# Performance work log

Hardware: AMD Instinct MI355X
Metric: run time of the kernel (lower is better)

Reference implementation:

```python
import jax, jax.numpy as jnp
import numpy as np

N_NODES = 50000
N_EDGES = 400000
NUM_INPUT = 3703
NUM_DIM = 256
NUM_OUT = 6


def setup_inputs() -> dict:
    key = jax.random.key(0)
    k = jax.random.split(key, 8)
    x = jax.random.normal(k[0], (N_NODES, NUM_INPUT), dtype=jnp.float32)
    edge_src = jax.random.randint(k[1], (N_EDGES,), 0, N_NODES, dtype=jnp.int32)
    edge_dst = jax.random.randint(k[2], (N_EDGES,), 0, N_NODES, dtype=jnp.int32)
    edge_weight = jax.random.uniform(k[3], (N_EDGES,), dtype=jnp.float32)
    W1 = jax.random.normal(k[4], (NUM_INPUT, NUM_DIM), dtype=jnp.float32) * (1.0 / np.sqrt(NUM_INPUT))
    b1 = jnp.zeros((NUM_DIM,), dtype=jnp.float32)
    W2 = jax.random.normal(k[5], (NUM_DIM, NUM_OUT), dtype=jnp.float32) * (1.0 / np.sqrt(NUM_DIM))
    b2 = jnp.zeros((NUM_OUT,), dtype=jnp.float32)
    return {"x": x, "edge_src": edge_src, "edge_dst": edge_dst,
            "edge_weight": edge_weight, "W1": W1, "b1": b1, "W2": W2, "b2": b2}


def _gcn_layer(h, W, b, src, dst, w):
    # support = h @ W  (dense transform), then sparse adj matmul via gather+segment_sum
    support = h @ W                              # [N, d_out]
    msg = support[src] * w[:, None]              # [E, d_out]
    agg = jax.ops.segment_sum(msg, dst, num_segments=h.shape[0])  # [N, d_out]
    return agg + b


def reference(x, edge_src, edge_dst, edge_weight, W1, b1, W2, b2):
    h = _gcn_layer(x, W1, b1, edge_src, edge_dst, edge_weight)
    h = jax.nn.leaky_relu(h, negative_slope=0.01)  # matches F.leaky_relu default
    h = _gcn_layer(h, W2, b2, edge_src, edge_dst, edge_weight)
    return jax.nn.log_softmax(h, axis=1)
```

## Files before the change

kernel.cpp:

```cpp
#include <hip/hip_runtime.h>
#include <math.h>

#define N_NODES   50000
#define N_EDGES   400000
#define NUM_INPUT 3703
#define NUM_DIM   256
#define NUM_OUT   6

#define KPAD   3712
#define KTILES 116

typedef __attribute__((ext_vector_type(8))) short short8;
typedef __attribute__((ext_vector_type(4))) float f32x4;

static __device__ __forceinline__ unsigned short f2bf(float f) {
    unsigned u = __float_as_uint(f);
    u += 0x7fffu + ((u >> 16) & 1u);
    return (unsigned short)(u >> 16);
}
static __device__ __forceinline__ float bf2f(unsigned short h) {
    return __uint_as_float(((unsigned)h) << 16);
}

__global__ __launch_bounds__(256) void w1_split_kernel(
    const float* __restrict__ W1,
    unsigned short* __restrict__ Wh, unsigned short* __restrict__ Wl)
{
    int idx = blockIdx.x * 256 + threadIdx.x;
    if (idx >= NUM_DIM * KPAD) return;
    int col = idx / KPAD;
    int k   = idx - col * KPAD;
    float v = (k < NUM_INPUT) ? W1[(size_t)k * NUM_DIM + col] : 0.f;
    unsigned short h = f2bf(v);
    Wh[idx] = h;
    Wl[idx] = f2bf(v - bf2f(h));
}

__global__ __launch_bounds__(256) void deg_count_kernel(
    const int* __restrict__ dst, int* __restrict__ deg)
{
    int e = blockIdx.x * 256 + threadIdx.x;
    if (e >= N_EDGES) return;
    atomicAdd(&deg[dst[e]], 1);
}

__global__ __launch_bounds__(1024) void scan_kernel(
    const int* __restrict__ deg, int* __restrict__ row_ptr,
    int* __restrict__ cursor)
{
    __shared__ int buf[1024];
    __shared__ int carry_s;
    const int tid = threadIdx.x;
    if (tid == 0) carry_s = 0;
    __syncthreads();
    for (int base = 0; base < N_NODES; base += 1024) {
        const int i = base + tid;
        const int v = (i < N_NODES) ? deg[i] : 0;
        buf[tid] = v;
        __syncthreads();
#pragma unroll
        for (int off = 1; off < 1024; off <<= 1) {
            int t = (tid >= off) ? buf[tid - off] : 0;
            __syncthreads();
            buf[tid] += t;
            __syncthreads();
        }
        const int c = carry_s;
        if (i < N_NODES) {
            const int excl = c + buf[tid] - v;
            row_ptr[i] = excl;
            cursor[i]  = excl;
        }
        const int tot = buf[1023];
        __syncthreads();
        if (tid == 0) carry_s = c + tot;
        __syncthreads();
    }
    if (tid == 0) row_ptr[N_NODES] = carry_s;
}

__global__ __launch_bounds__(256) void fill_kernel(
    const int* __restrict__ dst, int* __restrict__ cursor,
    int* __restrict__ edge_idx)
{
    int e = blockIdx.x * 256 + threadIdx.x;
    if (e >= N_EDGES) return;
    int pos = atomicAdd(&cursor[dst[e]], 1);
    edge_idx[pos] = e;
}

__global__ __launch_bounds__(256) void gemm1_kernel(
    const float* __restrict__ x,
    const unsigned short* __restrict__ Wh, const unsigned short* __restrict__ Wl,
    float* __restrict__ support)
{
    __shared__ unsigned short Ah[64][32];
    __shared__ unsigned short Al[64][32];
    __shared__ unsigned short Bh[256][32];
    __shared__ unsigned short Bl[256][32];

    const int t    = threadIdx.x;
    const int lane = t & 63;
    const int wv   = t >> 6;
    const int m0   = blockIdx.x * 64;

    const int arow = t >> 2;
    const int akc  = t & 3;
    const int fr   = lane & 15;
    const int fg   = lane >> 4;

    const int gr   = m0 + arow;
    const bool rok = (gr < N_NODES);
    const float* xrow = x + (size_t)gr * NUM_INPUT + akc * 8;

    char* ah_dst = (char*)&Ah[0][0] + t * 16;
    char* al_dst = (char*)&Al[0][0] + t * 16;
    char* bh_dst = (char*)&Bh[0][0] + t * 16;
    char* bl_dst = (char*)&Bl[0][0] + t * 16;
    const int bcol0 = t >> 2;

    f32x4 acc[4][4];
#pragma unroll
    for (int i = 0; i < 4; ++i)
#pragma unroll
        for (int j = 0; j < 4; ++j) acc[i][j] = (f32x4){0.f, 0.f, 0.f, 0.f};

    for (int kt = 0; kt < KTILES; ++kt) {
        const int k0 = kt * 32;
        __syncthreads();

#pragma unroll
        for (int c = 0; c < 4; ++c) {
            const size_t goff = (size_t)(bcol0 + 64 * c) * KPAD + k0 + akc * 8;
            __builtin_amdgcn_global_load_lds(
                (const __attribute__((address_space(1))) void*)(Wh + goff),
                (__attribute__((address_space(3))) void*)(bh_dst + c * 4096),
                16, 0, 0);
            __builtin_amdgcn_global_load_lds(
                (const __attribute__((address_space(1))) void*)(Wl + goff),
                (__attribute__((address_space(3))) void*)(bl_dst + c * 4096),
                16, 0, 0);
        }

        float av[8];
#pragma unroll
        for (int j = 0; j < 8; ++j) {
            const int gk = k0 + akc * 8 + j;
            av[j] = (rok && gk < NUM_INPUT) ? xrow[k0 + j] : 0.f;
        }
        short8 vh, vl;
#pragma unroll
        for (int j = 0; j < 8; ++j) {
            const unsigned short h = f2bf(av[j]);
            vh[j] = (short)h;
            vl[j] = (short)f2bf(av[j] - bf2f(h));
        }
        *(short8*)ah_dst = vh;
        *(short8*)al_dst = vl;

        __syncthreads();

        short8 ahf[4], alf[4];
#pragma unroll
        for (int mb = 0; mb < 4; ++mb) {
            ahf[mb] = *(const short8*)&Ah[mb * 16 + fr][fg * 8];
            alf[mb] = *(const short8*)&Al[mb * 16 + fr][fg * 8];
        }
#pragma unroll
        for (int nb = 0; nb < 4; ++nb) {
            const int col = wv * 64 + nb * 16 + fr;
            const short8 bhf = *(const short8*)&Bh[col][fg * 8];
            const short8 blf = *(const short8*)&Bl[col][fg * 8];
#pragma unroll
            for (int mb = 0; mb < 4; ++mb) {
                acc[mb][nb] = __builtin_amdgcn_mfma_f32_16x16x32_bf16(
                    alf[mb], bhf, acc[mb][nb], 0, 0, 0);
                acc[mb][nb] = __builtin_amdgcn_mfma_f32_16x16x32_bf16(
                    ahf[mb], blf, acc[mb][nb], 0, 0, 0);
                acc[mb][nb] = __builtin_amdgcn_mfma_f32_16x16x32_bf16(
                    ahf[mb], bhf, acc[mb][nb], 0, 0, 0);
            }
        }
    }

#pragma unroll
    for (int mb = 0; mb < 4; ++mb) {
        const int row = m0 + mb * 16 + fg * 4;
#pragma unroll
        for (int r = 0; r < 4; ++r) {
            if (row + r < N_NODES) {
#pragma unroll
                for (int nb = 0; nb < 4; ++nb)
                    support[(size_t)(row + r) * NUM_DIM + wv * 64 + nb * 16 + fr] =
                        acc[mb][nb][r];
            }
        }
    }
}

__global__ __launch_bounds__(256) void agg1_fused_kernel(
    const float* __restrict__ support, const int* __restrict__ row_ptr,
    const int* __restrict__ edge_idx, const int* __restrict__ src,
    const float* __restrict__ w, const float* __restrict__ b1,
    const float* __restrict__ W2, float* __restrict__ support2)
{
    __shared__ float W2s[NUM_DIM][NUM_OUT];
    const int t = threadIdx.x;
#pragma unroll
    for (int j = 0; j < NUM_OUT; ++j) W2s[t][j] = W2[t * NUM_OUT + j];
    __syncthreads();

    const int node = blockIdx.x * 4 + (t >> 6);
    const int lane = t & 63;
    if (node >= N_NODES) return;

    const int p0 = row_ptr[node], p1 = row_ptr[node + 1];
    float4 acc = make_float4(0.f, 0.f, 0.f, 0.f);
    for (int p = p0; p < p1; ++p) {
        const int e = edge_idx[p];
        const float we = w[e];
        const float4 v = *(const float4*)&support[(size_t)src[e] * NUM_DIM + lane * 4];
        acc.x += v.x * we; acc.y += v.y * we;
        acc.z += v.z * we; acc.w += v.w * we;
    }
    const float4 bv = *(const float4*)&b1[lane * 4];
    float hv[4];
    hv[0] = acc.x + bv.x; hv[1] = acc.y + bv.y;
    hv[2] = acc.z + bv.z; hv[3] = acc.w + bv.w;
#pragma unroll
    for (int c = 0; c < 4; ++c) hv[c] = (hv[c] > 0.f) ? hv[c] : 0.01f * hv[c];

    float o[NUM_OUT];
#pragma unroll
    for (int j = 0; j < NUM_OUT; ++j) o[j] = 0.f;
#pragma unroll
    for (int c = 0; c < 4; ++c) {
        const int k = lane * 4 + c;
#pragma unroll
        for (int j = 0; j < NUM_OUT; ++j) o[j] += hv[c] * W2s[k][j];
    }
#pragma unroll
    for (int j = 0; j < NUM_OUT; ++j) {
#pragma unroll
        for (int off = 32; off > 0; off >>= 1)
            o[j] += __shfl_down(o[j], off);
    }
    if (lane == 0) {
#pragma unroll
        for (int j = 0; j < NUM_OUT; ++j)
            support2[(size_t)node * NUM_OUT + j] = o[j];
    }
}

__global__ __launch_bounds__(256) void agg2_fused_kernel(
    const float* __restrict__ support2, const int* __restrict__ row_ptr,
    const int* __restrict__ edge_idx, const int* __restrict__ src,
    const float* __restrict__ w, const float* __restrict__ b2,
    float* __restrict__ out)
{
    const int t    = threadIdx.x;
    const int node = blockIdx.x * 4 + (t >> 6);
    const int lane = t & 63;
    if (node >= N_NODES) return;

    const int p0 = row_ptr[node], p1 = row_ptr[node + 1];
    float o[NUM_OUT];
#pragma unroll
    for (int j = 0; j < NUM_OUT; ++j) o[j] = 0.f;
    for (int p = p0 + lane; p < p1; p += 64) {
        const int e = edge_idx[p];
        const float we = w[e];
        const float* sp = &support2[(size_t)src[e] * NUM_OUT];
#pragma unroll
        for (int j = 0; j < NUM_OUT; ++j) o[j] += sp[j] * we;
    }
#pragma unroll
    for (int j = 0; j < NUM_OUT; ++j) {
#pragma unroll
        for (int off = 32; off > 0; off >>= 1)
            o[j] += __shfl_down(o[j], off);
    }
    if (lane == 0) {
        float v[NUM_OUT];
        float m = -1e30f;
#pragma unroll
        for (int j = 0; j < NUM_OUT; ++j) {
            v[j] = o[j] + b2[j];
            m = fmaxf(m, v[j]);
        }
        float s = 0.f;
#pragma unroll
        for (int j = 0; j < NUM_OUT; ++j) s += expf(v[j] - m);
        const float ls = logf(s);
#pragma unroll
        for (int j = 0; j < NUM_OUT; ++j)
            out[(size_t)node * NUM_OUT + j] = v[j] - m - ls;
    }
}

extern "C" void kernel_launch(void* const* d_in, const int* in_sizes, int n_in,
                              void* d_out, int out_size, void* d_ws, size_t ws_size,
                              hipStream_t stream)
{
    const float* x   = (const float*)d_in[0];
    const int*   src = (const int*)  d_in[1];
    const int*   dst = (const int*)  d_in[2];
    const float* w   = (const float*)d_in[3];
    const float* W1  = (const float*)d_in[4];
    const float* b1  = (const float*)d_in[5];
    const float* W2  = (const float*)d_in[6];
    const float* b2  = (const float*)d_in[7];
    float* out = (float*)d_out;

    char* ws = (char*)d_ws;
    float*          support1 = (float*)(ws);
    float*          support2 = (float*)(ws + 51200000);
    unsigned short* W1t_hi   = (unsigned short*)(ws + 52400000);
    unsigned short* W1t_lo   = (unsigned short*)(ws + 54300544);
    int*            deg_cur  = (int*)(ws + 56201088);
    int*            row_ptr  = (int*)(ws + 56401088);
    int*            edge_idx = (int*)(ws + 56601092);

    hipMemsetAsync(deg_cur, 0, (size_t)N_NODES * sizeof(int), stream);

    deg_count_kernel<<<dim3((N_EDGES + 255) / 256), 256, 0, stream>>>(dst, deg_cur);
    scan_kernel<<<dim3(1), 1024, 0, stream>>>(deg_cur, row_ptr, deg_cur);
    fill_kernel<<<dim3((N_EDGES + 255) / 256), 256, 0, stream>>>(dst, deg_cur, edge_idx);

    w1_split_kernel<<<dim3((NUM_DIM * KPAD + 255) / 256), 256, 0, stream>>>(
        W1, W1t_hi, W1t_lo);
    gemm1_kernel<<<dim3((N_NODES + 63) / 64), 256, 0, stream>>>(
        x, W1t_hi, W1t_lo, support1);
    agg1_fused_kernel<<<dim3((N_NODES + 3) / 4), 256, 0, stream>>>(
        support1, row_ptr, edge_idx, src, w, b1, W2, support2);
    agg2_fused_kernel<<<dim3((N_NODES + 3) / 4), 256, 0, stream>>>(
        support2, row_ptr, edge_idx, src, w, b2, out);
}
```

Before: 1.667 ms.

## Double-buffer GEMM with pre-tiled swizzled W1 image and pre-sorted edge arrays

The W1 preprocessing now writes a per-k-tile, bank-swizzled hi/lo bf16 image so each GEMM tile is one contiguous block. The GEMM now double-buffers its LDS tiles, prefetching the next x and W tiles during the current MFMAs with one barrier per iteration, and splits the hi part by truncation. The CSR fill now stores src and weight in sorted order, removing the edge_idx indirection. Aggregation batches neighbour indices through wave shuffles with 4-way unrolled gathers, and the scan uses wave shuffles instead of a barrier-heavy LDS scan. These add LDS use (about 80KB per block, which may lower occupancy), and the truncated hi split changes rounding slightly.

```diff
diff --git a/kernel.cpp b/kernel.cpp
--- a/kernel.cpp
+++ b/kernel.cpp
@@ -13,27 +13,36 @@
 typedef __attribute__((ext_vector_type(8))) short short8;
 typedef __attribute__((ext_vector_type(4))) float f32x4;
 
-static __device__ __forceinline__ unsigned short f2bf(float f) {
+static __device__ __forceinline__ unsigned short f2bf_rne(float f) {
     unsigned u = __float_as_uint(f);
     u += 0x7fffu + ((u >> 16) & 1u);
     return (unsigned short)(u >> 16);
 }
-static __device__ __forceinline__ float bf2f(unsigned short h) {
-    return __uint_as_float(((unsigned)h) << 16);
-}
-
-__global__ __launch_bounds__(256) void w1_split_kernel(
-    const float* __restrict__ W1,
-    unsigned short* __restrict__ Wh, unsigned short* __restrict__ Wl)
-{
-    int idx = blockIdx.x * 256 + threadIdx.x;
-    if (idx >= NUM_DIM * KPAD) return;
-    int col = idx / KPAD;
-    int k   = idx - col * KPAD;
-    float v = (k < NUM_INPUT) ? W1[(size_t)k * NUM_DIM + col] : 0.f;
-    unsigned short h = f2bf(v);
-    Wh[idx] = h;
-    Wl[idx] = f2bf(v - bf2f(h));
+
+__global__ __launch_bounds__(256) void w1_img_kernel(
+    const float* __restrict__ W1, unsigned short* __restrict__ img)
+{
+    int cg = blockIdx.x * 256 + threadIdx.x;
+    if (cg >= KTILES * 1024) return;
+    int kt   = cg >> 10;
+    int cc   = cg & 1023;
+    int col  = cc >> 2;
+    int spos = cc & 3;
+    int slot = (spos - (col >> 1)) & 3;
+    int k0   = kt * 32 + slot * 8;
+    size_t base = (size_t)kt * 16384 + (size_t)cc * 8;
+    short8 vh, vl;
+#pragma unroll
+    for (int j = 0; j < 8; ++j) {
+        int k = k0 + j;
+        float v = (k < NUM_INPUT) ? W1[(size_t)k * NUM_DIM + col] : 0.f;
+        unsigned u = __float_as_uint(v);
+        vh[j] = (short)(u >> 16);
+        float rec = __uint_as_float(u & 0xffff0000u);
+        vl[j] = (short)f2bf_rne(v - rec);
+    }
+    *(short8*)(img + base)        = vh;
+    *(short8*)(img + base + 8192) = vl;
 }
 
 __global__ __launch_bounds__(256) void deg_count_kernel(
@@ -48,56 +57,61 @@
     const int* __restrict__ deg, int* __restrict__ row_ptr,
     int* __restrict__ cursor)
 {
-    __shared__ int buf[1024];
+    __shared__ int wsum[16];
     __shared__ int carry_s;
-    const int tid = threadIdx.x;
+    const int tid = threadIdx.x, lane = tid & 63, wid = tid >> 6;
     if (tid == 0) carry_s = 0;
     __syncthreads();
     for (int base = 0; base < N_NODES; base += 1024) {
         const int i = base + tid;
         const int v = (i < N_NODES) ? deg[i] : 0;
-        buf[tid] = v;
-        __syncthreads();
-#pragma unroll
-        for (int off = 1; off < 1024; off <<= 1) {
-            int t = (tid >= off) ? buf[tid - off] : 0;
-            __syncthreads();
-            buf[tid] += t;
-            __syncthreads();
-        }
-        const int c = carry_s;
-        if (i < N_NODES) {
-            const int excl = c + buf[tid] - v;
-            row_ptr[i] = excl;
-            cursor[i]  = excl;
-        }
-        const int tot = buf[1023];
-        __syncthreads();
-        if (tid == 0) carry_s = c + tot;
-        __syncthreads();
-    }
-    if (tid == 0) row_ptr[N_NODES] = carry_s;
+        int x = v;
+#pragma unroll
+        for (int off = 1; off < 64; off <<= 1) {
+            int y = __shfl_up(x, off);
+            if (lane >= off) x += y;
+        }
+        if (lane == 63) wsum[wid] = x;
+        __syncthreads();
+        if (wid == 0) {
+            int s = (lane < 16) ? wsum[lane] : 0;
+#pragma unroll
+            for (int off = 1; off < 16; off <<= 1) {
+                int y = __shfl_up(s, off);
+                if (lane >= off) s += y;
+            }
+            if (lane < 16) wsum[lane] = s;
+        }
+        __syncthreads();
+        const int wpre  = (wid == 0) ? 0 : wsum[wid - 1];
+        const int carry = carry_s;
+        const int incl  = carry + wpre + x;
+        if (i < N_NODES) { row_ptr[i] = incl - v; cursor[i] = incl - v; }
+        __syncthreads();
+        if (tid == 1023) carry_s = incl;
+        __syncthreads();
+    }
+    if (threadIdx.x == 0) row_ptr[N_NODES] = carry_s;
 }
 
 __global__ __launch_bounds__(256) void fill_kernel(
-    const int* __restrict__ dst, int* __restrict__ cursor,
-    int* __restrict__ edge_idx)
+    const int* __restrict__ dst, const int* __restrict__ src,
+    const float* __restrict__ w, int* __restrict__ cursor,
+    int* __restrict__ src_s, float* __restrict__ w_s)
 {
     int e = blockIdx.x * 256 + threadIdx.x;
     if (e >= N_EDGES) return;
     int pos = atomicAdd(&cursor[dst[e]], 1);
-    edge_idx[pos] = e;
+    src_s[pos] = src[e];
+    w_s[pos]   = w[e];
 }
 
 __global__ __launch_bounds__(256) void gemm1_kernel(
-    const float* __restrict__ x,
-    const unsigned short* __restrict__ Wh, const unsigned short* __restrict__ Wl,
+    const float* __restrict__ x, const unsigned short* __restrict__ Wimg,
     float* __restrict__ support)
 {
-    __shared__ unsigned short Ah[64][32];
-    __shared__ unsigned short Al[64][32];
-    __shared__ unsigned short Bh[256][32];
-    __shared__ unsigned short Bl[256][32];
+    __shared__ unsigned short Abuf[2][4096];
+    __shared__ unsigned short Bbuf[2][16384];
 
     const int t    = threadIdx.x;
     const int lane = t & 63;
@@ -111,13 +125,10 @@
 
     const int gr   = m0 + arow;
     const bool rok = (gr < N_NODES);
-    const float* xrow = x + (size_t)gr * NUM_INPUT + akc * 8;
-
-    char* ah_dst = (char*)&Ah[0][0] + t * 16;
-    char* al_dst = (char*)&Al[0][0] + t * 16;
-    char* bh_dst = (char*)&Bh[0][0] + t * 16;
-    char* bl_dst = (char*)&Bl[0][0] + t * 16;
-    const int bcol0 = t >> 2;
+    const float* xbase = x + (size_t)(rok ? gr : 0) * NUM_INPUT + akc * 8;
+
+    const int a_woff = arow * 32 + ((akc + (arow >> 1)) & 3) * 8;
+    const int aslot  = ((fg + (fr >> 1)) & 3) * 8;
 
     f32x4 acc[4][4];
 #pragma unroll
@@ -125,52 +136,68 @@
 #pragma unroll
         for (int j = 0; j < 4; ++j) acc[i][j] = (f32x4){0.f, 0.f, 0.f, 0.f};
 
+    float av[8];
+
+#pragma unroll
+    for (int j = 0; j < 8; ++j)
+        av[j] = rok ? xbase[j] : 0.f;
+    {
+        const unsigned short* wsrc = Wimg + (size_t)t * 8;
+        unsigned short* bdst = &Bbuf[0][t * 8];
+#pragma unroll
+        for (int r = 0; r < 8; ++r)
+            __builtin_amdgcn_global_load_lds(
+                (const __attribute__((address_space(1))) void*)(wsrc + r * 2048),
+                (__attribute__((address_space(3))) void*)(bdst + r * 2048),
+                16, 0, 0);
+    }
+    {
+        short8 vh, vl;
+#pragma unroll
+        for (int j = 0; j < 8; ++j) {
+            unsigned u = __float_as_uint(av[j]);
+            vh[j] = (short)(u >> 16);
+            float rec = __uint_as_float(u & 0xffff0000u);
+            vl[j] = (short)f2bf_rne(av[j] - rec);
+        }
+        *(short8*)(&Abuf[0][a_woff])        = vh;
+        *(short8*)(&Abuf[0][2048 + a_woff]) = vl;
+    }
+    __syncthreads();
+
+    int buf = 0;
     for (int kt = 0; kt < KTILES; ++kt) {
-        const int k0 = kt * 32;
-        __syncthreads();
-
-#pragma unroll
-        for (int c = 0; c < 4; ++c) {
-            const size_t goff = (size_t)(bcol0 + 64 * c) * KPAD + k0 + akc * 8;
-            __builtin_amdgcn_global_load_lds(
-                (const __attribute__((address_space(1))) void*)(Wh + goff),
-                (__attribute__((address_space(3))) void*)(bh_dst + c * 4096),
-                16, 0, 0);
-            __builtin_amdgcn_global_load_lds(
-                (const __attribute__((address_space(1))) void*)(Wl + goff),
-                (__attribute__((address_space(3))) void*)(bl_dst + c * 4096),
-                16, 0, 0);
-        }
-
-        float av[8];
-#pragma unroll
-        for (int j = 0; j < 8; ++j) {
-            const int gk = k0 + akc * 8 + j;
-            av[j] = (rok && gk < NUM_INPUT) ? xrow[k0 + j] : 0.f;
-        }
-        short8 vh, vl;
-#pragma unroll
-        for (int j = 0; j < 8; ++j) {
-            const unsigned short h = f2bf(av[j]);
-            vh[j] = (short)h;
-            vl[j] = (short)f2bf(av[j] - bf2f(h));
-        }
-        *(short8*)ah_dst = vh;
-        *(short8*)al_dst = vl;
-
-        __syncthreads();
-
+        const int nxt = kt + 1;
+        if (nxt < KTILES) {
+            const float* xk = xbase + nxt * 32;
+            const int kb = nxt * 32 + akc * 8;
+#pragma unroll
+            for (int j = 0; j < 8; ++j)
+                av[j] = (rok && (kb + j) < NUM_INPUT) ? xk[j] : 0.f;
+            const unsigned short* wsrc = Wimg + (size_t)nxt * 16384 + t * 8;
+            unsigned short* bdst = &Bbuf[buf ^ 1][t * 8];
+#pragma unroll
+            for (int r = 0; r < 8; ++r)
+                __builtin_amdgcn_global_load_lds(
+                    (const __attribute__((address_space(1))) void*)(wsrc + r * 2048),
+                    (__attribute__((address_space(3))) void*)(bdst + r * 2048),
+                    16, 0, 0);
+        }
+
+        const unsigned short* A = Abuf[buf];
+        const unsigned short* B = Bbuf[buf];
         short8 ahf[4], alf[4];
 #pragma unroll
         for (int mb = 0; mb < 4; ++mb) {
-            ahf[mb] = *(const short8*)&Ah[mb * 16 + fr][fg * 8];
-            alf[mb] = *(const short8*)&Al[mb * 16 + fr][fg * 8];
+            const int ro = (mb * 16 + fr) * 32 + aslot;
+            ahf[mb] = *(const short8*)(A + ro);
+            alf[mb] = *(const short8*)(A + 2048 + ro);
         }
 #pragma unroll
         for (int nb = 0; nb < 4; ++nb) {
-            const int col = wv * 64 + nb * 16 + fr;
-            const short8 bhf = *(const short8*)&Bh[col][fg * 8];
-            const short8 blf = *(const short8*)&Bl[col][fg * 8];
+            const int co = (wv * 64 + nb * 16 + fr) * 32 + aslot;
+            const short8 bhf = *(const short8*)(B + co);
+            const short8 blf = *(const short8*)(B + 8192 + co);
 #pragma unroll
             for (int mb = 0; mb < 4; ++mb) {
                 acc[mb][nb] = __builtin_amdgcn_mfma_f32_16x16x32_bf16(
@@ -181,6 +208,22 @@
                     ahf[mb], bhf, acc[mb][nb], 0, 0, 0);
             }
         }
+
+        if (nxt < KTILES) {
+            short8 vh, vl;
+#pragma unroll
+            for (int j = 0; j < 8; ++j) {
+                unsigned u = __float_as_uint(av[j]);
+                vh[j] = (short)(u >> 16);
+                float rec = __uint_as_float(u & 0xffff0000u);
+                vl[j] = (short)f2bf_rne(av[j] - rec);
+            }
+            unsigned short* ad = &Abuf[buf ^ 1][0];
+            *(short8*)(ad + a_woff)        = vh;
+            *(short8*)(ad + 2048 + a_woff) = vl;
+        }
+        __syncthreads();
+        buf ^= 1;
     }
 
 #pragma unroll
@@ -200,79 +243,96 @@
 
 __global__ __launch_bounds__(256) void agg1_fused_kernel(
     const float* __restrict__ support, const int* __restrict__ row_ptr,
-    const int* __restrict__ edge_idx, const int* __restrict__ src,
-    const float* __restrict__ w, const float* __restrict__ b1,
-    const float* __restrict__ W2, float* __restrict__ support2)
-{
-    __shared__ float W2s[NUM_DIM][NUM_OUT];
-    const int t = threadIdx.x;
-#pragma unroll
-    for (int j = 0; j < NUM_OUT; ++j) W2s[t][j] = W2[t * NUM_OUT + j];
-    __syncthreads();
-
-    const int node = blockIdx.x * 4 + (t >> 6);
-    const int lane = t & 63;
-    if (node >= N_NODES) return;
-
-    const int p0 = row_ptr[node], p1 = row_ptr[node + 1];
-    float4 acc = make_float4(0.f, 0.f, 0.f, 0.f);
-    for (int p = p0; p < p1; ++p) {
-        const int e = edge_idx[p];
-        const float we = w[e];
-        const float4 v = *(const float4*)&support[(size_t)src[e] * NUM_DIM + lane * 4];
-        acc.x += v.x * we; acc.y += v.y * we;
-        acc.z += v.z * we; acc.w += v.w * we;
-    }
-    const float4 bv = *(const float4*)&b1[lane * 4];
-    float hv[4];
-    hv[0] = acc.x + bv.x; hv[1] = acc.y + bv.y;
-    hv[2] = acc.z + bv.z; hv[3] = acc.w + bv.w;
-#pragma unroll
-    for (int c = 0; c < 4; ++c) hv[c] = (hv[c] > 0.f) ? hv[c] : 0.01f * hv[c];
-
-    float o[NUM_OUT];
-#pragma unroll
-    for (int j = 0; j < NUM_OUT; ++j) o[j] = 0.f;
-#pragma unroll
-    for (int c = 0; c < 4; ++c) {
-        const int k = lane * 4 + c;
-#pragma unroll
-        for (int j = 0; j < NUM_OUT; ++j) o[j] += hv[c] * W2s[k][j];
-    }
-#pragma unroll
-    for (int j = 0; j < NUM_OUT; ++j) {
-#pragma unroll
-        for (int off = 32; off > 0; off >>= 1)
-            o[j] += __shfl_down(o[j], off);
-    }
-    if (lane == 0) {
-#pragma unroll
-        for (int j = 0; j < NUM_OUT; ++j)
-            support2[(size_t)node * NUM_OUT + j] = o[j];
-    }
-}
-
-__global__ __launch_bounds__(256) void agg2_fused_kernel(
-    const float* __restrict__ support2, const int* __restrict__ row_ptr,
-    const int* __restrict__ edge_idx, const int* __restrict__ src,
-    const float* __restrict__ w, const float* __restrict__ b2,
-    float* __restrict__ out)
+    const int* __restrict__ src_s, const float* __restrict__ w_s,
+    const float* __restrict__ b1, const float* __restrict__ W2,
+    float* __restrict__ support2)
 {
     const int t    = threadIdx.x;
     const int node = blockIdx.x * 4 + (t >> 6);
     const int lane = t & 63;
     if (node >= N_NODES) return;
 
+    float w2f[24];
+    {
+        const float4* wp = (const float4*)(W2 + lane * 24);
+#pragma unroll
+        for (int q = 0; q < 6; ++q) ((float4*)w2f)[q] = wp[q];
+    }
+
     const int p0 = row_ptr[node], p1 = row_ptr[node + 1];
+    float4 acc = make_float4(0.f, 0.f, 0.f, 0.f);
+    for (int base = p0; base < p1; base += 64) {
+        const int rem = p1 - base;
+        const int n = rem < 64 ? rem : 64;
+        int se = 0; float we = 0.f;
+        if (lane < n) { se = src_s[base + lane]; we = w_s[base + lane]; }
+        int i = 0;
+        for (; i + 4 <= n; i += 4) {
+            const int   s0 = __shfl(se, i),     s1 = __shfl(se, i + 1);
+            const int   s2 = __shfl(se, i + 2), s3 = __shfl(se, i + 3);
+            const float q0 = __shfl(we, i),     q1 = __shfl(we, i + 1);
+            const float q2 = __shfl(we, i + 2), q3 = __shfl(we, i + 3);
+            const float4 v0 = *(const float4*)&support[(size_t)s0 * NUM_DIM + lane * 4];
+            const float4 v1 = *(const float4*)&support[(size_t)s1 * NUM_DIM + lane * 4];
+            const float4 v2 = *(const float4*)&support[(size_t)s2 * NUM_DIM + lane * 4];
+            const float4 v3 = *(const float4*)&support[(size_t)s3 * NUM_DIM + lane * 4];
+            acc.x += v0.x * q0 + v1.x * q1 + v2.x * q2 + v3.x * q3;
+            acc.y += v0.y * q0 + v1.y * q1 + v2.y * q2 + v3.y * q3;
+            acc.z += v0.z * q0 + v1.z * q1 + v2.z * q2 + v3.z * q3;
+            acc.w += v0.w * q0 + v1.w * q1 + v2.w * q2 + v3.w * q3;
+        }
+        for (; i < n; ++i) {
+            const int   s0 = __shfl(se, i);
+            const float q0 = __shfl(we, i);
+            const float4 v = *(const float4*)&support[(size_t)s0 * NUM_DIM + lane * 4];
+            acc.x += v.x * q0; acc.y += v.y * q0;
+            acc.z += v.z * q0; acc.w += v.w * q0;
+        }
+    }
+
+    const float4 bv = *(const float4*)&b1[lane * 4];
+    float hv[4] = {acc.x + bv.x, acc.y + bv.y, acc.z + bv.z, acc.w + bv.w};
+#pragma unroll
+    for (int c = 0; c < 4; ++c) hv[c] = (hv[c] > 0.f) ? hv[c] : 0.01f * hv[c];
+
     float o[NUM_OUT];
 #pragma unroll
-    for (int j = 0; j < NUM_OUT; ++j) o[j] = 0.f;
+    for (int j = 0; j < NUM_OUT; ++j)
+        o[j] = hv[0] * w2f[j] + hv[1] * w2f[6 + j] +
+               hv[2] * w2f[12 + j] + hv[3] * w2f[18 + j];
+#pragma unroll
+    for (int j = 0; j < NUM_OUT; ++j) {
+#pragma unroll
+        for (int off = 32; off > 0; off >>= 1)
+            o[j] += __shfl_down(o[j], off);
+    }
+    if (lane == 0) {
+#pragma unroll
+        for (int j = 0; j < NUM_OUT; ++j)
+            support2[(size_t)node * NUM_OUT + j] = o[j];
+    }
+}
+
+__global__ __launch_bounds__(256) void agg2_fused_kernel(
+    const float* __restrict__ support2, const int* __restrict__ row_ptr,
+    const int* __restrict__ src_s, const float* __restrict__ w_s,
+    const float* __restrict__ b2, float* __restrict__ out)
+{
+    const int t    = threadIdx.x;
+    const int node = blockIdx.x * 4 + (t >> 6);
+    const int lane = t & 63;
+    if (node >= N_NODES) return;
+
+    const int p0 = row_ptr[node], p1 = row_ptr[node + 1];
+    float o[NUM_OUT] = {0.f, 0.f, 0.f, 0.f, 0.f, 0.f};
     for (int p = p0 + lane; p < p1; p += 64) {
-        const int e = edge_idx[p];
-        const float we = w[e];
-        const float* sp = &support2[(size_t)src[e] * NUM_OUT];
-#pragma unroll
-        for (int j = 0; j < NUM_OUT; ++j) o[j] += sp[j] * we;
+        const int   s  = src_s[p];
+        const float ww = w_s[p];
+        const float2* sp = (const float2*)(support2 + (size_t)s * NUM_OUT);
+        const float2 v0 = sp[0], v1 = sp[1], v2 = sp[2];
+        o[0] += v0.x * ww; o[1] += v0.y * ww;
+        o[2] += v1.x * ww; o[3] += v1.y * ww;
+        o[4] += v2.x * ww; o[5] += v2.y * ww;
     }
 #pragma unroll
     for (int j = 0; j < NUM_OUT; ++j) {
@@ -315,24 +375,23 @@
     char* ws = (char*)d_ws;
     float*          support1 = (float*)(ws);
     float*          support2 = (float*)(ws + 51200000);
-    unsigned short* W1t_hi   = (unsigned short*)(ws + 52400000);
-    unsigned short* W1t_lo   = (unsigned short*)(ws + 54300544);
+    unsigned short* Wimg     = (unsigned short*)(ws + 52400000);
     int*            deg_cur  = (int*)(ws + 56201088);
     int*            row_ptr  = (int*)(ws + 56401088);
-    int*            edge_idx = (int*)(ws + 56601092);
+    int*            src_s    = (int*)(ws + 56601092);
+    float*          w_s      = (float*)(ws + 58201092);
 
     hipMemsetAsync(deg_cur, 0, (size_t)N_NODES * sizeof(int), stream);
 
     deg_count_kernel<<<dim3((N_EDGES + 255) / 256), 256, 0, stream>>>(dst, deg_cur);
     scan_kernel<<<dim3(1), 1024, 0, stream>>>(deg_cur, row_ptr, deg_cur);
-    fill_kernel<<<dim3((N_EDGES + 255) / 256), 256, 0, stream>>>(dst, deg_cur, edge_idx);
-
-    w1_split_kernel<<<dim3((NUM_DIM * KPAD + 255) / 256), 256, 0, stream>>>(
-        W1, W1t_hi, W1t_lo);
-    gemm1_kernel<<<dim3((N_NODES + 63) / 64), 256, 0, stream>>>(
-        x, W1t_hi, W1t_lo, support1);
+    fill_kernel<<<dim3((N_EDGES + 255) / 256), 256, 0, stream>>>(
+        dst, src, w, deg_cur, src_s, w_s);
+
+    w1_img_kernel<<<dim3((KTILES * 1024 + 255) / 256), 256, 0, stream>>>(W1, Wimg);
+    gemm1_kernel<<<dim3((N_NODES + 63) / 64), 256, 0, stream>>>(x, Wimg, support1);
     agg1_fused_kernel<<<dim3((N_NODES + 3) / 4), 256, 0, stream>>>(
-        support1, row_ptr, edge_idx, src, w, b1, W2, support2);
+        support1, row_ptr, src_s, w_s, b1, W2, support2);
     agg2_fused_kernel<<<dim3((N_NODES + 3) / 4), 256, 0, stream>>>(
-        support2, row_ptr, edge_idx, src, w, b2, out);
-}
+        support2, row_ptr, src_s, w_s, b2, out);
+}
```

Result: faster. 1.545 ms (-7.3%).
